# Kernel optimization log

Hardware: AMD Instinct MI355X
Metric: run time of the kernel (lower is better)

The kernel has to match this reference:

```python
import jax, jax.numpy as jnp
import numpy as np

D_MODEL, N_HEADS, D_FF = 512, 8, 2048
D_K = D_MODEL // N_HEADS
EPS = 1e-5


def layer_norm(x, g, b):
    mu = jnp.mean(x, axis=-1, keepdims=True)
    var = jnp.mean(jnp.square(x - mu), axis=-1, keepdims=True)
    return (x - mu) * jax.lax.rsqrt(var + EPS) * g + b


def setup_inputs() -> dict:
    key = jax.random.key(0)
    ks = jax.random.split(key, 12)
    B, S = 2, 2048
    s_attn = 1.0 / np.sqrt(D_MODEL)
    s_ff1 = 1.0 / np.sqrt(D_MODEL)
    s_ff2 = 1.0 / np.sqrt(D_FF)
    inp = {
        "x": jax.random.normal(ks[0], (B, S, D_MODEL), dtype=jnp.float32),
        "mask": jnp.ones((B, 1, 1, S), dtype=jnp.int32),
        "Wq": jax.random.normal(ks[1], (D_MODEL, D_MODEL), jnp.float32) * s_attn,
        "bq": jnp.zeros((D_MODEL,), jnp.float32),
        "Wk": jax.random.normal(ks[2], (D_MODEL, D_MODEL), jnp.float32) * s_attn,
        "bk": jnp.zeros((D_MODEL,), jnp.float32),
        "Wv": jax.random.normal(ks[3], (D_MODEL, D_MODEL), jnp.float32) * s_attn,
        "bv": jnp.zeros((D_MODEL,), jnp.float32),
        "Wo": jax.random.normal(ks[4], (D_MODEL, D_MODEL), jnp.float32) * s_attn,
        "bo": jnp.zeros((D_MODEL,), jnp.float32),
        "W1": jax.random.normal(ks[5], (D_MODEL, D_FF), jnp.float32) * s_ff1,
        "b1": jnp.zeros((D_FF,), jnp.float32),
        "W2": jax.random.normal(ks[6], (D_FF, D_MODEL), jnp.float32) * s_ff2,
        "b2": jnpp.zeros((D_MODEL,), jnp.float32) if False else jnp.zeros((D_MODEL,), jnp.float32),
        "g1": jnp.ones((D_MODEL,), jnp.float32),
        "beta1": jnp.zeros((D_MODEL,), jnp.float32),
        "g2": jnp.ones((D_MODEL,), jnp.float32),
        "beta2": jnp.zeros((D_MODEL,), jnp.float32),
    }
    return inp


def reference(x, mask, Wq, bq, Wk, bk, Wv, bv, Wo, bo, W1, b1, W2, b2, g1, beta1, g2, beta2):
    B, S, _ = x.shape
    # projections -> [B, H, S, Dk]
    def split_heads(t):
        return t.reshape(B, S, N_HEADS, D_K).transpose(0, 2, 1, 3)
    q = split_heads(x @ Wq + bq)
    k = split_heads(x @ Wk + bk)
    v = split_heads(x @ Wv + bv)
    scores = jnp.einsum("bhqd,bhkd->bhqk", q, k) / np.sqrt(D_K)
    scores = jnp.where(mask == 0, jnp.float32(-1e9), scores)
    attn = jax.nn.softmax(scores, axis=-1)
    ctx = jnp.einsum("bhqk,bhkd->bhqd", attn, v)
    ctx = ctx.transpose(0, 2, 1, 3).reshape(B, S, D_MODEL)
    attn_out = ctx @ Wo + bo
    x1 = layer_norm(x + attn_out, g1, beta1)
    ff = jax.nn.relu(x1 @ W1 + b1) @ W2 + b2
    return layer_norm(x1 + ff, g2, beta2)
```

## Files before the change

### kernel.cpp

```cpp
#include <hip/hip_runtime.h>
#include <hip/hip_bf16.h>


#define D_MODEL 512
#define N_HEADS 8
#define D_K 64
#define D_FF 2048
#define BATCH 2
#define SEQ 2048
#define NROWS (BATCH * SEQ)

typedef __hip_bfloat16 bf16;
typedef __attribute__((ext_vector_type(8))) short bf16x8;
typedef __attribute__((ext_vector_type(4))) float f32x4;

__device__ __forceinline__ unsigned short f2b(float f) {
  union { bf16 b; unsigned short u; } cv;
  cv.b = __float2bfloat16(f);
  return cv.u;
}
__device__ __forceinline__ float b2f(unsigned short u) {
  return __uint_as_float(((unsigned int)u) << 16);
}
__device__ __forceinline__ float toF(const bf16 x) { return __bfloat162float(x); }
__device__ __forceinline__ float toF(const float x) { return x; }
__device__ __forceinline__ void storeC(float* p, float v) { *p = v; }
__device__ __forceinline__ void storeC(bf16* p, float v) {
  *p = __float2bfloat16(v);
}

__device__ __forceinline__ void dma16(const void* g, void* l) {
  __builtin_amdgcn_global_load_lds(
      (const __attribute__((address_space(1))) unsigned int*)g,
      (__attribute__((address_space(3))) unsigned int*)l, 16, 0, 0);
}

__device__ __forceinline__ void ld8f(const float* p, float* v) {
  const float4 a = *(const float4*)p;
  const float4 b = *(const float4*)(p + 4);
  v[0] = a.x; v[1] = a.y; v[2] = a.z; v[3] = a.w;
  v[4] = b.x; v[5] = b.y; v[6] = b.z; v[7] = b.w;
}
__device__ __forceinline__ void ld8f(const bf16* p, float* v) {
  const bf16x8 u = *(const bf16x8*)p;
#pragma unroll
  for (int i = 0; i < 8; ++i) v[i] = b2f((unsigned short)u[i]);
}
__device__ __forceinline__ void st8f(float* p, const float* v) {
  *(float4*)p = make_float4(v[0], v[1], v[2], v[3]);
  *(float4*)(p + 4) = make_float4(v[4], v[5], v[6], v[7]);
}
__device__ __forceinline__ void st8f(bf16* p, const float* v) {
  bf16x8 u;
#pragma unroll
  for (int i = 0; i < 8; ++i) u[i] = (short)f2b(v[i]);
  *(bf16x8*)p = u;
}

#define WT_Q 0
#define WT_K 262144
#define WT_V 524288
#define WT_O 786432
#define WT_1 1048576
#define WT_2 2097152

__global__ __launch_bounds__(256) void prep_kernel(
    const float* __restrict__ Wq, const float* __restrict__ Wk,
    const float* __restrict__ Wv, const float* __restrict__ Wo,
    const float* __restrict__ W1, const float* __restrict__ W2,
    bf16* __restrict__ outw, const float* __restrict__ x,
    bf16* __restrict__ xb) {
  const int z = blockIdx.z;
  const int t = threadIdx.x;

  if (z == 6) {
    const size_t base =
        ((size_t)(blockIdx.y * 32 + blockIdx.x) * 2048) + (size_t)t * 8;
    float v[8];
    ld8f(x + base, v);
    st8f(xb + base, v);
    return;
  }

  const float* W;
  int R, Cn;
  size_t off;
  if (z == 0)      { W = Wq; R = 512;  Cn = 512;  off = WT_Q; }
  else if (z == 1) { W = Wk; R = 512;  Cn = 512;  off = WT_K; }
  else if (z == 2) { W = Wv; R = 512;  Cn = 512;  off = WT_V; }
  else if (z == 3) { W = Wo; R = 512;  Cn = 512;  off = WT_O; }
  else if (z == 4) { W = W1; R = 512;  Cn = 2048; off = WT_1; }
  else             { W = W2; R = 2048; Cn = 512;  off = WT_2; }
  const int c0 = blockIdx.x * 64;
  const int r0 = blockIdx.y * 64;
  if (c0 >= Cn || r0 >= R) return;

  __shared__ short tile[64][72];
  {
    const int r = t >> 2, cg = (t & 3) * 16;
    const float* src = &W[(size_t)(r0 + r) * Cn + c0 + cg];
#pragma unroll
    for (int i = 0; i < 4; ++i) {
      const float4 v = *(const float4*)(src + 4 * i);
      tile[cg + 4 * i + 0][r] = (short)f2b(v.x);
      tile[cg + 4 * i + 1][r] = (short)f2b(v.y);
      tile[cg + 4 * i + 2][r] = (short)f2b(v.z);
      tile[cg + 4 * i + 3][r] = (short)f2b(v.w);
    }
  }
  __syncthreads();
  {
    const int c = t >> 2, rg = (t & 3) * 16;
    short* dst = (short*)outw + off + (size_t)(c0 + c) * R + r0 + rg;
    *(bf16x8*)dst = *(const bf16x8*)&tile[c][rg];
    *(bf16x8*)(dst + 8) = *(const bf16x8*)&tile[c][rg + 8];
  }
}

template <int BM, bool RELU, bool RESID>
__global__ __launch_bounds__(256) void gemm_bf16_kernel(
    const bf16* __restrict__ A, int lda,
    const bf16* __restrict__ Wt0, const bf16* __restrict__ Wt1,
    const bf16* __restrict__ Wt2, int ldk,
    const float* __restrict__ b0, const float* __restrict__ b1,
    const float* __restrict__ b2,
    bf16* __restrict__ C0, bf16* __restrict__ C1, bf16* __restrict__ C2,
    int ldc, int K, const bf16* __restrict__ R) {
  const bf16* Wt = (blockIdx.z == 0) ? Wt0 : (blockIdx.z == 1 ? Wt1 : Wt2);
  const float* bias = (blockIdx.z == 0) ? b0 : (blockIdx.z == 1 ? b1 : b2);
  bf16* C = (blockIdx.z == 0) ? C0 : (blockIdx.z == 1 ? C1 : C2);

  constexpr int RG = BM / 64;
  constexpr int AI = BM / 32;
  constexpr int RSH = (BM == 64) ? 6 : 7;

  __shared__ __align__(16) short asA[8 * BM * 8];
  __shared__ __align__(16) short bsW[8 * 64 * 8];

  const int rowBase = blockIdx.y * BM;
  const int colBase = blockIdx.x * 64;
  const int t = threadIdx.x;
  const int wave = t >> 6;
  const int lane = t & 63;
  const int quad = lane >> 4;
  const int l15 = lane & 15;

  f32x4 acc[RG][4];
#pragma unroll
  for (int i = 0; i < RG; ++i)
#pragma unroll
    for (int nt = 0; nt < 4; ++nt) acc[i][nt] = (f32x4){0.f, 0.f, 0.f, 0.f};

  for (int k0 = 0; k0 < K; k0 += 64) {
#pragma unroll
    for (int i = 0; i < AI; ++i) {
      const int s = (wave * AI + i) * 64 + lane;
      const int c = s >> RSH;
      const int row = s & (BM - 1);
      dma16((const short*)A + (size_t)(rowBase + row) * lda + k0 + c * 8,
            (char*)asA + (size_t)(wave * AI + i) * 1024);
    }
#pragma unroll
    for (int i = 0; i < 2; ++i) {
      const int s = (wave * 2 + i) * 64 + lane;
      const int c = s >> 6;
      const int row = s & 63;
      dma16((const short*)Wt + (size_t)(colBase + row) * ldk + k0 + c * 8,
            (char*)bsW + (size_t)(wave * 2 + i) * 1024);
    }
    __syncthreads();

#pragma unroll
    for (int kc = 0; kc < 2; ++kc) {
      bf16x8 af[RG];
#pragma unroll
      for (int i = 0; i < RG; ++i)
        af[i] = *(const bf16x8*)
            &asA[((quad + 4 * kc) * BM + wave * (16 * RG) + i * 16 + l15) * 8];
#pragma unroll
      for (int nt = 0; nt < 4; ++nt) {
        const bf16x8 bfr =
            *(const bf16x8*)&bsW[((quad + 4 * kc) * 64 + nt * 16 + l15) * 8];
#pragma unroll
        for (int i = 0; i < RG; ++i)
          acc[i][nt] = __builtin_amdgcn_mfma_f32_16x16x32_bf16(
              af[i], bfr, acc[i][nt], 0, 0, 0);
      }
    }
    __syncthreads();
  }

#pragma unroll
  for (int i = 0; i < RG; ++i)
#pragma unroll
    for (int nt = 0; nt < 4; ++nt) {
      const int col = colBase + nt * 16 + l15;
#pragma unroll
      for (int r = 0; r < 4; ++r) {
        const int row = rowBase + wave * (16 * RG) + i * 16 + quad * 4 + r;
        float v = acc[i][nt][r] + bias[col];
        if (RESID) v += toF(R[(size_t)row * ldc + col]);
        if (RELU) v = fmaxf(v, 0.f);
        storeC(&C[(size_t)row * ldc + col], v);
      }
    }
}

__global__ __launch_bounds__(512) void attn_mfma_kernel(
    const bf16* __restrict__ Q, const bf16* __restrict__ Km,
    const bf16* __restrict__ V, const int* __restrict__ mask,
    bf16* __restrict__ ctx) {
  const int qt = blockIdx.x;
  const int bh = blockIdx.y;
  const int b = bh >> 3;
  const int h = bh & 7;
  const int t = threadIdx.x;
  const int wave = t >> 6;
  const int half = wave >> 2;
  const int wq = wave & 3;
  const int lane = t & 63;
  const int quad = lane >> 4;
  const int l15 = lane & 15;

  __shared__ __align__(16) char smem[74240];
  auto ks = (short(*)[64][72])(smem);
  auto vt = (short(*)[64][72])(smem + 18432);
  auto pb = (short(*)[32][72])(smem + 36864);
  auto mk = (int(*)[64])(smem + 73728);
  auto mg = (float(*)[32][68])(smem);

  bf16x8 qf[2][2];
#pragma unroll
  for (int rg = 0; rg < 2; ++rg) {
    const short* qg = (const short*)Q +
        (size_t)(b * SEQ + qt * 128 + wq * 32 + rg * 16 + l15) * D_MODEL +
        h * D_K + quad * 8;
    qf[rg][0] = *(const bf16x8*)qg;
    qf[rg][1] = *(const bf16x8*)(qg + 32);
  }

  f32x4 of[2][4];
#pragma unroll
  for (int rg = 0; rg < 2; ++rg)
#pragma unroll
    for (int nt = 0; nt < 4; ++nt) of[rg][nt] = (f32x4){0.f, 0.f, 0.f, 0.f};
  float l_acc[2][4] = {{0.f, 0.f, 0.f, 0.f}, {0.f, 0.f, 0.f, 0.f}};

  const int hs = t >> 8;
  const int tt = t & 255;
  const int kr = tt >> 2, kc0 = (tt & 3) * 16;
  const int vk = tt & 63, vc0 = ((tt >> 6) & 3) * 16;

  bf16x8 kv0, kv1, vv0, vv1;
  int mv = 1;
  {
    const int keyRow = (hs * 16 + 0) * 64;
    const short* kg = (const short*)Km +
        (size_t)(b * SEQ + keyRow + kr) * D_MODEL + h * D_K + kc0;
    kv0 = *(const bf16x8*)kg;
    kv1 = *(const bf16x8*)(kg + 8);
    const short* vg = (const short*)V +
        (size_t)(b * SEQ + keyRow + vk) * D_MODEL + h * D_K + vc0;
    vv0 = *(const bf16x8*)vg;
    vv1 = *(const bf16x8*)(vg + 8);
    if (tt < 64) mv = mask[b * SEQ + keyRow + tt];
  }

  for (int kt = 0; kt < 16; ++kt) {
    *(bf16x8*)&ks[hs][kr][kc0] = kv0;
    *(bf16x8*)&ks[hs][kr][kc0 + 8] = kv1;
#pragma unroll
    for (int i = 0; i < 8; ++i) vt[hs][vc0 + i][vk] = vv0[i];
#pragma unroll
    for (int i = 0; i < 8; ++i) vt[hs][vc0 + 8 + i][vk] = vv1[i];
    if (tt < 64) mk[hs][tt] = mv;

    if (kt + 1 < 16) {
      const int keyRow = (hs * 16 + kt + 1) * 64;
      const short* kg = (const short*)Km +
          (size_t)(b * SEQ + keyRow + kr) * D_MODEL + h * D_K + kc0;
      kv0 = *(const bf16x8*)kg;
      kv1 = *(const bf16x8*)(kg + 8);
      const short* vg = (const short*)V +
          (size_t)(b * SEQ + keyRow + vk) * D_MODEL + h * D_K + vc0;
      vv0 = *(const bf16x8*)vg;
      vv1 = *(const bf16x8*)(vg + 8);
      if (tt < 64) mv = mask[b * SEQ + keyRow + tt];
    }
    __syncthreads();

    f32x4 sf[2][4];
#pragma unroll
    for (int nt = 0; nt < 4; ++nt) {
      const bf16x8 kf0 = *(const bf16x8*)&ks[half][l15 + 16 * nt][quad * 8];
      const bf16x8 kf1 =
          *(const bf16x8*)&ks[half][l15 + 16 * nt][quad * 8 + 32];
#pragma unroll
      for (int rg = 0; rg < 2; ++rg) {
        f32x4 acc = (f32x4){0.f, 0.f, 0.f, 0.f};
        acc = __builtin_amdgcn_mfma_f32_16x16x32_bf16(qf[rg][0], kf0, acc, 0, 0, 0);
        acc = __builtin_amdgcn_mfma_f32_16x16x32_bf16(qf[rg][1], kf1, acc, 0, 0, 0);
        sf[rg][nt] = acc;
      }
    }

#pragma unroll
    for (int nt = 0; nt < 4; ++nt) {
      const bool dead = (mk[half][l15 + 16 * nt] == 0);
#pragma unroll
      for (int rg = 0; rg < 2; ++rg)
#pragma unroll
        for (int r = 0; r < 4; ++r) {
          float p = __expf(fmaf(sf[rg][nt][r], 0.125f, -8.f));
          if (dead) p = 0.f;
          l_acc[rg][r] += p;
          pb[wave][rg * 16 + quad * 4 + r][l15 + 16 * nt] = (short)f2b(p);
        }
    }

#pragma unroll
    for (int kc = 0; kc < 2; ++kc) {
      bf16x8 pf[2];
#pragma unroll
      for (int rg = 0; rg < 2; ++rg)
        pf[rg] = *(const bf16x8*)&pb[wave][rg * 16 + l15][kc * 32 + quad * 8];
#pragma unroll
      for (int nt = 0; nt < 4; ++nt) {
        const bf16x8 vf =
            *(const bf16x8*)&vt[half][l15 + 16 * nt][kc * 32 + quad * 8];
#pragma unroll
        for (int rg = 0; rg < 2; ++rg)
          of[rg][nt] = __builtin_amdgcn_mfma_f32_16x16x32_bf16(
              pf[rg], vf, of[rg][nt], 0, 0, 0);
      }
    }
    __syncthreads();
  }

#pragma unroll
  for (int xm = 1; xm < 16; xm <<= 1)
#pragma unroll
    for (int rg = 0; rg < 2; ++rg)
#pragma unroll
      for (int r = 0; r < 4; ++r)
        l_acc[rg][r] += __shfl_xor(l_acc[rg][r], xm, 64);

#pragma unroll
  for (int rg = 0; rg < 2; ++rg)
#pragma unroll
    for (int nt = 0; nt < 4; ++nt)
#pragma unroll
      for (int r = 0; r < 4; ++r)
        mg[wave][rg * 16 + quad * 4 + r][l15 + 16 * nt] = of[rg][nt][r];
  if (l15 == 0) {
#pragma unroll
    for (int rg = 0; rg < 2; ++rg)
#pragma unroll
      for (int r = 0; r < 4; ++r)
        mg[wave][rg * 16 + quad * 4 + r][64] = l_acc[rg][r];
  }
  __syncthreads();

  if (wave < 4) {
    const int pw = wave + 4;
#pragma unroll
    for (int rg = 0; rg < 2; ++rg)
#pragma unroll
      for (int r = 0; r < 4; ++r) {
        const int qrow = rg * 16 + quad * 4 + r;
        const float inv = 1.f / (l_acc[rg][r] + mg[pw][qrow][64]);
        const int row = qt * 128 + wave * 32 + qrow;
        bf16* cp = ctx + (size_t)(b * SEQ + row) * D_MODEL + h * D_K;
#pragma unroll
        for (int nt = 0; nt < 4; ++nt)
          cp[l15 + 16 * nt] = __float2bfloat16(
              (of[rg][nt][r] + mg[pw][qrow][l15 + 16 * nt]) * inv);
      }
  }
}

template <typename BT, typename OT>
__global__ __launch_bounds__(256) void ln_kernel(
    const BT* __restrict__ base, const float* __restrict__ g,
    const float* __restrict__ beta, OT* __restrict__ out) {
  const int wave = threadIdx.x >> 6;
  const int lane = threadIdx.x & 63;
  const int row = blockIdx.x * 4 + wave;
  const size_t rb = (size_t)row * D_MODEL + lane * 8;

  float v[8];
  ld8f(base + rb, v);

  float s = 0.f;
#pragma unroll
  for (int i = 0; i < 8; ++i) s += v[i];
#pragma unroll
  for (int xm = 1; xm < 64; xm <<= 1) s += __shfl_xor(s, xm, 64);
  const float mu = s * (1.f / (float)D_MODEL);

  float q = 0.f;
#pragma unroll
  for (int i = 0; i < 8; ++i) {
    v[i] -= mu;
    q += v[i] * v[i];
  }
#pragma unroll
  for (int xm = 1; xm < 64; xm <<= 1) q += __shfl_xor(q, xm, 64);
  const float rs = rsqrtf(q * (1.f / (float)D_MODEL) + 1e-5f);

  float gv[8], bv[8];
  ld8f(g + lane * 8, gv);
  ld8f(beta + lane * 8, bv);
#pragma unroll
  for (int i = 0; i < 8; ++i) v[i] = v[i] * rs * gv[i] + bv[i];
  st8f(out + rb, v);
}

extern "C" void kernel_launch(void* const* d_in, const int* in_sizes, int n_in,
                              void* d_out, int out_size, void* d_ws, size_t ws_size,
                              hipStream_t stream) {
  const float* x     = (const float*)d_in[0];
  const int*   mask  = (const int*)d_in[1];
  const float* Wq    = (const float*)d_in[2];
  const float* bq    = (const float*)d_in[3];
  const float* Wk    = (const float*)d_in[4];
  const float* bk    = (const float*)d_in[5];
  const float* Wv    = (const float*)d_in[6];
  const float* bv    = (const float*)d_in[7];
  const float* Wo    = (const float*)d_in[8];
  const float* bo    = (const float*)d_in[9];
  const float* W1    = (const float*)d_in[10];
  const float* b1    = (const float*)d_in[11];
  const float* W2    = (const float*)d_in[12];
  const float* b2    = (const float*)d_in[13];
  const float* g1    = (const float*)d_in[14];
  const float* beta1 = (const float*)d_in[15];
  const float* g2    = (const float*)d_in[16];
  const float* beta2 = (const float*)d_in[17];
  float* out = (float*)d_out;

  char* ws = (char*)d_ws;
  const size_t MB4 = (size_t)NROWS * D_MODEL * sizeof(bf16);
  bf16* q        = (bf16*)(ws + 0 * MB4);
  bf16* kbuf     = (bf16*)(ws + 1 * MB4);
  bf16* vbuf     = (bf16*)(ws + 2 * MB4);
  bf16* ctx      = (bf16*)(ws + 3 * MB4);
  bf16* xb       = (bf16*)(ws + 4 * MB4);
  bf16* attn_out = q;
  bf16* x1       = kbuf;
  bf16* ffacc    = vbuf;
  bf16* ffmid    = (bf16*)(ws + 4 * MB4);

  bf16* wt = (bf16*)d_out;

  const dim3 blk(256);

  prep_kernel<<<dim3(32, 32, 7), blk, 0, stream>>>(Wq, Wk, Wv, Wo, W1, W2, wt,
                                                   x, xb);

  gemm_bf16_kernel<128, false, false>
      <<<dim3(D_MODEL / 64, NROWS / 128, 3), blk, 0, stream>>>(
          xb, D_MODEL, wt + WT_Q, wt + WT_K, wt + WT_V, D_MODEL,
          bq, bk, bv, q, kbuf, vbuf, D_MODEL, D_MODEL, nullptr);

  attn_mfma_kernel<<<dim3(SEQ / 128, BATCH * N_HEADS), dim3(512), 0, stream>>>(
      q, kbuf, vbuf, mask, ctx);

  gemm_bf16_kernel<64, false, true>
      <<<dim3(D_MODEL / 64, NROWS / 64, 1), blk, 0, stream>>>(
          ctx, D_MODEL, wt + WT_O, wt + WT_O, wt + WT_O, D_MODEL,
          bo, bo, bo, attn_out, attn_out, attn_out, D_MODEL, D_MODEL, xb);

  ln_kernel<bf16, bf16><<<NROWS / 4, blk, 0, stream>>>(attn_out, g1, beta1, x1);

  gemm_bf16_kernel<128, true, false>
      <<<dim3(D_FF / 64, NROWS / 128, 1), blk, 0, stream>>>(
          x1, D_MODEL, wt + WT_1, wt + WT_1, wt + WT_1, D_MODEL,
          b1, b1, b1, ffmid, ffmid, ffmid, D_FF, D_MODEL, nullptr);

  gemm_bf16_kernel<64, false, true>
      <<<dim3(D_MODEL / 64, NROWS / 64, 1), blk, 0, stream>>>(
          ffmid, D_FF, wt + WT_2, wt + WT_2, wt + WT_2, D_FF,
          b2, b2, b2, ffacc, ffacc, ffacc, D_MODEL, D_FF, x1);

  ln_kernel<bf16, float><<<NROWS / 4, blk, 0, stream>>>(ffacc, g2, beta2, out);
}
```

Measured before the change: 245.3 us.

## Double-buffer GEMM tiles with register prefetch instead of global_load_lds DMA

Replaces the direct global-to-LDS DMA loads in the bf16 GEMM with register-staged loads that prefetch the next K tile while the current one is computed. LDS tiles are double-buffered, which removes the trailing barrier in each iteration. This aims to overlap global memory latency with MFMA work, at the cost of extra VGPRs for staging and twice the shared memory.

```diff
diff --git a/kernel.cpp b/kernel.cpp
--- a/kernel.cpp
+++ b/kernel.cpp
@@ -27,12 +27,6 @@
 __device__ __forceinline__ void storeC(float* p, float v) { *p = v; }
 __device__ __forceinline__ void storeC(bf16* p, float v) {
   *p = __float2bfloat16(v);
-}
-
-__device__ __forceinline__ void dma16(const void* g, void* l) {
-  __builtin_amdgcn_global_load_lds(
-      (const __attribute__((address_space(1))) unsigned int*)g,
-      (__attribute__((address_space(3))) unsigned int*)l, 16, 0, 0);
 }
 
 __device__ __forceinline__ void ld8f(const float* p, float* v) {
@@ -131,11 +125,11 @@
   bf16* C = (blockIdx.z == 0) ? C0 : (blockIdx.z == 1 ? C1 : C2);
 
   constexpr int RG = BM / 64;
-  constexpr int AI = BM / 32;
+  constexpr int NA = BM / 32;
   constexpr int RSH = (BM == 64) ? 6 : 7;
 
-  __shared__ __align__(16) short asA[8 * BM * 8];
-  __shared__ __align__(16) short bsW[8 * 64 * 8];
+  __shared__ __align__(16) short asA[2][8 * BM * 8];
+  __shared__ __align__(16) short bsW[2][8 * 64 * 8];
 
   const int rowBase = blockIdx.y * BM;
   const int colBase = blockIdx.x * 64;
@@ -145,28 +139,51 @@
   const int quad = lane >> 4;
   const int l15 = lane & 15;
 
+  const short* gA[NA];
+#pragma unroll
+  for (int i = 0; i < NA; ++i) {
+    const int s = i * 256 + t;
+    const int c = s >> RSH;
+    const int row = s & (BM - 1);
+    gA[i] = (const short*)A + (size_t)(rowBase + row) * lda + c * 8;
+  }
+  const short* gW[2];
+#pragma unroll
+  for (int i = 0; i < 2; ++i) {
+    const int s = i * 256 + t;
+    const int c = s >> 6;
+    const int row = s & 63;
+    gW[i] = (const short*)Wt + (size_t)(colBase + row) * ldk + c * 8;
+  }
+
+  bf16x8 areg[NA], wreg[2];
+#pragma unroll
+  for (int i = 0; i < NA; ++i) areg[i] = *(const bf16x8*)(gA[i]);
+#pragma unroll
+  for (int i = 0; i < 2; ++i) wreg[i] = *(const bf16x8*)(gW[i]);
+
   f32x4 acc[RG][4];
 #pragma unroll
   for (int i = 0; i < RG; ++i)
 #pragma unroll
     for (int nt = 0; nt < 4; ++nt) acc[i][nt] = (f32x4){0.f, 0.f, 0.f, 0.f};
 
+  int cur = 0;
   for (int k0 = 0; k0 < K; k0 += 64) {
 #pragma unroll
-    for (int i = 0; i < AI; ++i) {
-      const int s = (wave * AI + i) * 64 + lane;
-      const int c = s >> RSH;
-      const int row = s & (BM - 1);
-      dma16((const short*)A + (size_t)(rowBase + row) * lda + k0 + c * 8,
-            (char*)asA + (size_t)(wave * AI + i) * 1024);
-    }
-#pragma unroll
-    for (int i = 0; i < 2; ++i) {
-      const int s = (wave * 2 + i) * 64 + lane;
-      const int c = s >> 6;
-      const int row = s & 63;
-      dma16((const short*)Wt + (size_t)(colBase + row) * ldk + k0 + c * 8,
-            (char*)bsW + (size_t)(wave * 2 + i) * 1024);
+    for (int i = 0; i < NA; ++i)
+      *(bf16x8*)&asA[cur][(i * 256 + t) * 8] = areg[i];
+#pragma unroll
+    for (int i = 0; i < 2; ++i)
+      *(bf16x8*)&bsW[cur][(i * 256 + t) * 8] = wreg[i];
+
+    if (k0 + 64 < K) {
+#pragma unroll
+      for (int i = 0; i < NA; ++i)
+        areg[i] = *(const bf16x8*)(gA[i] + k0 + 64);
+#pragma unroll
+      for (int i = 0; i < 2; ++i)
+        wreg[i] = *(const bf16x8*)(gW[i] + k0 + 64);
     }
     __syncthreads();
 
@@ -176,18 +193,18 @@
 #pragma unroll
       for (int i = 0; i < RG; ++i)
         af[i] = *(const bf16x8*)
-            &asA[((quad + 4 * kc) * BM + wave * (16 * RG) + i * 16 + l15) * 8];
+            &asA[cur][((quad + 4 * kc) * BM + wave * (16 * RG) + i * 16 + l15) * 8];
 #pragma unroll
       for (int nt = 0; nt < 4; ++nt) {
-        const bf16x8 bfr =
-            *(const bf16x8*)&bsW[((quad + 4 * kc) * 64 + nt * 16 + l15) * 8];
+        const bf16x8 bfr = *(const bf16x8*)
+            &bsW[cur][((quad + 4 * kc) * 64 + nt * 16 + l15) * 8];
 #pragma unroll
         for (int i = 0; i < RG; ++i)
           acc[i][nt] = __builtin_amdgcn_mfma_f32_16x16x32_bf16(
               af[i], bfr, acc[i][nt], 0, 0, 0);
       }
     }
-    __syncthreads();
+    cur ^= 1;
   }
 
 #pragma unroll
```

New measurement: 246.3 us. Within noise of the previous version (+0.4%).
